# Kernel optimization log

Hardware: AMD Instinct MI355X
Metric: run time of the kernel (lower is better)

## Reference

```python
import jax, jax.numpy as jnp
import numpy as np

N_NODES = 50000
N_EDGES = 1600000
N_GRAPHS = 128
DIM_IN = 128
DIM_SELF = 16


def setup_inputs() -> dict:
    key = jax.random.key(0)
    ks = jax.random.split(key, 12)
    feat = jax.random.normal(ks[0], (N_NODES, DIM_IN), dtype=jnp.float32)
    self_feat = jax.random.normal(ks[1], (N_GRAPHS, DIM_SELF), dtype=jnp.float32)
    src = jax.random.randint(ks[2], (N_EDGES,), 0, N_NODES)
    dst = jax.random.randint(ks[3], (N_EDGES,), 0, N_NODES)
    graph_id = jnp.sort(jax.random.randint(ks[4], (N_NODES,), 0, N_GRAPHS))
    def lin(k, fan_in, fan_out):
        bound = 1.0 / np.sqrt(fan_in)
        return jax.random.uniform(k, (fan_in, fan_out), dtype=jnp.float32, minval=-bound, maxval=bound)
    W1 = lin(ks[5], DIM_IN, 100)
    b1 = jnp.zeros((100,), jnp.float32)
    W2 = lin(ks[6], 100, 20)
    b2 = jnp.zeros((20,), jnp.float32)
    Wf1 = lin(ks[7], 20 + DIM_SELF, 10)
    bf1 = jnp.zeros((10,), jnp.float32)
    Wf2 = lin(ks[8], 10, 1)
    bf2 = jnp.zeros((1,), jnp.float32)
    return {"feat": feat, "self_feat": self_feat, "src": src, "dst": dst,
            "graph_id": graph_id, "W1": W1, "b1": b1, "W2": W2, "b2": b2,
            "Wf1": Wf1, "bf1": bf1, "Wf2": Wf2, "bf2": bf2}


def _gcn_layer(h, src, dst, deg, W, b):
    # copy_u gather over edges + mean segment reduce over dst, then linear apply
    msg_sum = jax.ops.segment_sum(h[src], dst, num_segments=h.shape[0])  # [N, d]
    mean = msg_sum / jnp.maximum(deg, 1.0)[:, None]
    # DGL update_all leaves zero-in-degree nodes with their prior feature
    h_agg = jnp.where((deg > 0)[:, None], mean, h)
    return h_agg @ W + b


def reference(feat, self_feat, src, dst, graph_id, W1, b1, W2, b2, Wf1, bf1, Wf2, bf2):
    n = feat.shape[0]
    deg = jax.ops.segment_sum(jnp.ones((src.shape[0],), feat.dtype), dst, num_segments=n)
    h = jax.nn.relu(_gcn_layer(feat, src, dst, deg, W1, b1))   # [N,100]
    h = jax.nn.relu(_gcn_layer(h, src, dst, deg, W2, b2))      # [N,20]
    # dgl.mean_nodes: per-graph mean of node features
    g_sum = jax.ops.segment_sum(h, graph_id, num_segments=N_GRAPHS)  # [G,20]
    g_cnt = jax.ops.segment_sum(jnp.ones((n,), h.dtype), graph_id, num_segments=N_GRAPHS)
    hg = g_sum / jnp.maximum(g_cnt, 1.0)[:, None]
    fused = jnp.concatenate([hg, self_feat], axis=1)           # [G, 20+dim_self]
    out = jax.nn.relu(fused @ Wf1 + bf1) @ Wf2 + bf2           # [G, dim_out]
    return out
```

## Files before the change

kernel.cpp:

```cpp
#include <hip/hip_runtime.h>

constexpr int NN = 50000;
constexpr int NE = 1600000;
constexpr int NG = 128;
constexpr int BSTRIDE = 96;

constexpr int FILL_PASSES = 8;
constexpr int NODES_PER_PASS = 6250;
constexpr int BLOCKS_PER_PASS = (NE + 255) / 256;

constexpr int G1M_BLOCKS = (NN + 63) / 64;

constexpr int A1_NODES = 16;
constexpr int A1_BLOCKS = NN / A1_NODES;
constexpr int A2_BLOCKS = NN / 16;

#define OFF_CNT      0
#define OFF_GSUM     200000
#define OFF_GCNT     210240
#define ZERO_BYTES   210752
#define OFF_ADJ      210752
#define OFF_X1F      9810816
#define OFF_X2B      16210816

typedef float v2f __attribute__((ext_vector_type(2)));
typedef short bf16x8 __attribute__((ext_vector_type(8)));
typedef float f32x4 __attribute__((ext_vector_type(4)));

__device__ __forceinline__ unsigned short f2bf(float x) {
    unsigned int v = __float_as_uint(x);
    return (unsigned short)((v + 0x7FFFu + ((v >> 16) & 1u)) >> 16);
}
__device__ __forceinline__ float bflo(unsigned int u) { return __uint_as_float(u << 16); }
__device__ __forceinline__ float bfhi(unsigned int u) { return __uint_as_float(u & 0xFFFF0000u); }

__global__ void k_fill(const int* __restrict__ src, const int* __restrict__ dst,
                       int* __restrict__ cnt, unsigned short* __restrict__ adj) {
    const int pass = blockIdx.x & 7;
    const int chunk = blockIdx.x >> 3;
    const int i = chunk * 256 + threadIdx.x;
    if (i >= NE) return;
    const int d = dst[i];
    const int lo = pass * NODES_PER_PASS;
    if (d >= lo && d < lo + NODES_PER_PASS) {
        const int p = atomicAdd(&cnt[d], 1);
        if (p < BSTRIDE) adj[d * BSTRIDE + p] = (unsigned short)src[i];
    }
}

__global__ __launch_bounds__(256) void k_gemm1m(const float* __restrict__ feat,
                                                const float* __restrict__ W1,
                                                unsigned int* __restrict__ X1f) {
    const int t = threadIdx.x;
    const int wv = t >> 6;
    const int l  = t & 63;
    const int ln16 = l & 15;
    const int lh   = l >> 4;
    const int node = blockIdx.x * 64 + wv * 16 + ln16;
    const bool live = (node < NN);

    bf16x8 bfr[4];
#pragma unroll
    for (int ks = 0; ks < 4; ++ks) {
        float4 f0 = {0.f,0.f,0.f,0.f}, f1 = {0.f,0.f,0.f,0.f};
        if (live) {
            f0 = *(const float4*)(feat + node * 128 + ks * 32 + lh * 8);
            f1 = *(const float4*)(feat + node * 128 + ks * 32 + lh * 8 + 4);
        }
        bf16x8 b;
        b[0] = (short)f2bf(f0.x); b[1] = (short)f2bf(f0.y);
        b[2] = (short)f2bf(f0.z); b[3] = (short)f2bf(f0.w);
        b[4] = (short)f2bf(f1.x); b[5] = (short)f2bf(f1.y);
        b[6] = (short)f2bf(f1.z); b[7] = (short)f2bf(f1.w);
        bfr[ks] = b;
    }

#pragma unroll
    for (int ct = 0; ct < 7; ++ct) {
        const int col = ct * 16 + ln16;
        f32x4 acc = {0.f, 0.f, 0.f, 0.f};
#pragma unroll
        for (int ks = 0; ks < 4; ++ks) {
            bf16x8 a;
#pragma unroll
            for (int j = 0; j < 8; ++j) {
                const int k = ks * 32 + lh * 8 + j;
                a[j] = (col < 100) ? (short)f2bf(W1[k * 100 + col]) : (short)0;
            }
            acc = __builtin_amdgcn_mfma_f32_16x16x32_bf16(a, bfr[ks], acc, 0, 0, 0);
        }
        if (live) {
            int u = 0;
            u = __builtin_amdgcn_cvt_pk_fp8_f32(acc[0], acc[1], u, false);
            u = __builtin_amdgcn_cvt_pk_fp8_f32(acc[2], acc[3], u, true);
            X1f[node * 32 + ct * 4 + lh] = (unsigned int)u;
        }
    }
    if (live) X1f[node * 32 + 28 + lh] = 0u;
}

__global__ __launch_bounds__(256) void k_agg1g2(
        const uint4* __restrict__ X1u, const int* __restrict__ cnt,
        const unsigned short* __restrict__ adj, const float* __restrict__ b1,
        const float* __restrict__ W2, unsigned int* __restrict__ X2b) {
    __shared__ float hl[A1_NODES * 100];
    __shared__ float w2s[100 * 20];
    const int t = threadIdx.x;
    const int node0 = blockIdx.x * A1_NODES;
    for (int i = t; i < 2000; i += 256) w2s[i] = W2[i];

    const int nl   = t >> 4;
    const int l    = t & 15;
    const int q    = l & 7;
    const int half = l >> 3;
    const int node = node0 + nl;
    const int d = cnt[node];
    const unsigned short* ab = adj + node * BSTRIDE;
    float a[16];
#pragma unroll
    for (int j = 0; j < 16; ++j) a[j] = 0.f;

#define ACC4(UU, B) { v2f l_ = __builtin_amdgcn_cvt_pk_f32_fp8((int)(UU), false); \
                      v2f h_ = __builtin_amdgcn_cvt_pk_f32_fp8((int)(UU), true);  \
                      a[B+0] += l_.x; a[B+1] += l_.y; a[B+2] += h_.x; a[B+3] += h_.y; }
#define SET4(UU, B) { v2f l_ = __builtin_amdgcn_cvt_pk_f32_fp8((int)(UU), false); \
                      v2f h_ = __builtin_amdgcn_cvt_pk_f32_fp8((int)(UU), true);  \
                      a[B+0] = l_.x; a[B+1] = l_.y; a[B+2] = h_.x; a[B+3] = h_.y; }
#define ACCU4(U) ACC4((U).x, 0) ACC4((U).y, 4) ACC4((U).z, 8) ACC4((U).w, 12)

    if (q < 7) {
        if (d == 0) {
            if (half == 0) {
                const uint4 u = X1u[node * 8 + q];
                SET4(u.x, 0) SET4(u.y, 4) SET4(u.z, 8) SET4(u.w, 12)
            }
        } else {
            const int m  = (d >> 1) & ~3;
            const int i0 = half ? m : 0;
            const int i1 = half ? d : m;
            int i = i0;
            for (; i + 8 <= i1; i += 8) {
                const ushort4 sa = *(const ushort4*)(ab + i);
                const ushort4 sb = *(const ushort4*)(ab + i + 4);
                const uint4 u0 = X1u[(int)sa.x * 8 + q];
                const uint4 u1 = X1u[(int)sa.y * 8 + q];
                const uint4 u2 = X1u[(int)sa.z * 8 + q];
                const uint4 u3 = X1u[(int)sa.w * 8 + q];
                const uint4 u4 = X1u[(int)sb.x * 8 + q];
                const uint4 u5 = X1u[(int)sb.y * 8 + q];
                const uint4 u6 = X1u[(int)sb.z * 8 + q];
                const uint4 u7 = X1u[(int)sb.w * 8 + q];
                ACCU4(u0) ACCU4(u1) ACCU4(u2) ACCU4(u3)
                ACCU4(u4) ACCU4(u5) ACCU4(u6) ACCU4(u7)
            }
            for (; i + 4 <= i1; i += 4) {
                const ushort4 s4 = *(const ushort4*)(ab + i);
                const uint4 u0 = X1u[(int)s4.x * 8 + q];
                const uint4 u1 = X1u[(int)s4.y * 8 + q];
                const uint4 u2 = X1u[(int)s4.z * 8 + q];
                const uint4 u3 = X1u[(int)s4.w * 8 + q];
                ACCU4(u0) ACCU4(u1) ACCU4(u2) ACCU4(u3)
            }
            for (; i < i1; ++i) {
                const uint4 u = X1u[(int)ab[i] * 8 + q];
                ACCU4(u)
            }
        }
    }
#undef ACCU4
#undef ACC4
#undef SET4
#pragma unroll
    for (int j = 0; j < 16; ++j) a[j] += __shfl_xor(a[j], 8);

    if (half == 0 && q < 7) {
        if (d > 0) {
            const float inv = 1.f / (float)d;
#pragma unroll
            for (int j = 0; j < 16; ++j) a[j] *= inv;
        }
        const int col0 = 16 * q;
        float* hrow = hl + nl * 100 + col0;
        const int nc = (q < 6) ? 16 : 4;
#pragma unroll 4
        for (int j = 0; j < nc; ++j)
            hrow[j] = fmaxf(a[j] + b1[col0 + j], 0.f);
    }
    __syncthreads();

    const int nl2 = t >> 4;
    const int j = t & 15;
    unsigned int o = 0u;
    if (j < 10) {
        const float* h = hl + nl2 * 100;
        float a0 = 0.f, a1 = 0.f;
#pragma unroll 5
        for (int k = 0; k < 100; ++k) {
            const float hv = h[k];
            a0 += hv * w2s[k * 20 + 2 * j];
            a1 += hv * w2s[k * 20 + 2 * j + 1];
        }
        o = (unsigned int)f2bf(a0) | ((unsigned int)f2bf(a1) << 16);
    }
    X2b[(node0 + nl2) * 16 + j] = o;
}

__global__ __launch_bounds__(256) void k_agg2(const uint2* __restrict__ X2v,
                                              const int* __restrict__ cnt,
                                              const unsigned short* __restrict__ adj,
                                              const float* __restrict__ b2,
                                              const int* __restrict__ graph_id,
                                              float* __restrict__ g_sum,
                                              float* __restrict__ g_cnt) {
    __shared__ float lsum[NG * 20];
    __shared__ float lcnt[NG];
    const int t = threadIdx.x;
    for (int i = t; i < NG * 20; i += 256) lsum[i] = 0.f;
    if (t < NG) lcnt[t] = 0.f;
    __syncthreads();

    const int nl   = t >> 4;
    const int l    = t & 15;
    const int q    = l & 7;
    const int half = l >> 3;
    const int node = blockIdx.x * 16 + nl;
    const int d = cnt[node];
    const unsigned short* ab = adj + node * BSTRIDE;
    float ax = 0.f, ay = 0.f, az = 0.f, aw = 0.f;
#define ACCU2(U) { ax += bflo((U).x); ay += bfhi((U).x); \
                   az += bflo((U).y); aw += bfhi((U).y); }
    if (q < 5) {
        if (d == 0) {
            if (half == 0) {
                const uint2 u = X2v[node * 8 + q];
                ax = bflo(u.x); ay = bfhi(u.x);
                az = bflo(u.y); aw = bfhi(u.y);
            }
        } else {
            const int m  = (d >> 1) & ~3;
            const int i0 = half ? m : 0;
            const int i1 = half ? d : m;
            int i = i0;
            for (; i + 8 <= i1; i += 8) {
                const ushort4 sa = *(const ushort4*)(ab + i);
                const ushort4 sb = *(const ushort4*)(ab + i + 4);
                const uint2 u0 = X2v[(int)sa.x * 8 + q];
                const uint2 u1 = X2v[(int)sa.y * 8 + q];
                const uint2 u2 = X2v[(int)sa.z * 8 + q];
                const uint2 u3 = X2v[(int)sa.w * 8 + q];
                const uint2 u4 = X2v[(int)sb.x * 8 + q];
                const uint2 u5 = X2v[(int)sb.y * 8 + q];
                const uint2 u6 = X2v[(int)sb.z * 8 + q];
                const uint2 u7 = X2v[(int)sb.w * 8 + q];
                ACCU2(u0) ACCU2(u1) ACCU2(u2) ACCU2(u3)
                ACCU2(u4) ACCU2(u5) ACCU2(u6) ACCU2(u7)
            }
            for (; i + 4 <= i1; i += 4) {
                const ushort4 s4 = *(const ushort4*)(ab + i);
                const uint2 u0 = X2v[(int)s4.x * 8 + q];
                const uint2 u1 = X2v[(int)s4.y * 8 + q];
                const uint2 u2 = X2v[(int)s4.z * 8 + q];
                const uint2 u3 = X2v[(int)s4.w * 8 + q];
                ACCU2(u0) ACCU2(u1) ACCU2(u2) ACCU2(u3)
            }
            for (; i < i1; ++i) {
                const uint2 u = X2v[(int)ab[i] * 8 + q];
                ACCU2(u)
            }
        }
    }
#undef ACCU2
    ax += __shfl_xor(ax, 8);
    ay += __shfl_xor(ay, 8);
    az += __shfl_xor(az, 8);
    aw += __shfl_xor(aw, 8);

    if (half == 0 && q < 5) {
        if (d > 0) {
            const float inv = 1.f / (float)d;
            ax *= inv; ay *= inv; az *= inv; aw *= inv;
        }
        const int col0 = 4 * q;
        const float hx = fmaxf(ax + b2[col0 + 0], 0.f);
        const float hy = fmaxf(ay + b2[col0 + 1], 0.f);
        const float hz = fmaxf(az + b2[col0 + 2], 0.f);
        const float hw = fmaxf(aw + b2[col0 + 3], 0.f);
        const int g = graph_id[node];
        atomicAdd(&lsum[g * 20 + col0 + 0], hx);
        atomicAdd(&lsum[g * 20 + col0 + 1], hy);
        atomicAdd(&lsum[g * 20 + col0 + 2], hz);
        atomicAdd(&lsum[g * 20 + col0 + 3], hw);
    }
    if (l == 0) atomicAdd(&lcnt[graph_id[node]], 1.f);
    __syncthreads();

    const int first = blockIdx.x * 16;
    const int gmin = graph_id[first];
    const int span = graph_id[first + 15] - gmin + 1;
    for (int idx = t; idx < span * 20; idx += 256) {
        const int g = gmin + idx / 20;
        const int c = idx - (idx / 20) * 20;
        const float v = lsum[g * 20 + c];
        if (v != 0.f) atomicAdd(&g_sum[g * 20 + c], v);
    }
    for (int idx = t; idx < span; idx += 256) {
        const float v = lcnt[gmin + idx];
        if (v != 0.f) atomicAdd(&g_cnt[gmin + idx], v);
    }
}

__global__ __launch_bounds__(128) void k_final(const float* __restrict__ g_sum,
                                               const float* __restrict__ g_cnt,
                                               const float* __restrict__ self_feat,
                                               const float* __restrict__ Wf1,
                                               const float* __restrict__ bf1,
                                               const float* __restrict__ Wf2,
                                               const float* __restrict__ bf2,
                                               float* __restrict__ out) {
    const int g = threadIdx.x;
    float fused[36];
    const float cnt = fmaxf(g_cnt[g], 1.f);
    const float inv = 1.f / cnt;
#pragma unroll
    for (int j = 0; j < 20; ++j) fused[j] = g_sum[g * 20 + j] * inv;
#pragma unroll
    for (int j = 0; j < 16; ++j) fused[20 + j] = self_feat[g * 16 + j];
    float o = bf2[0];
#pragma unroll
    for (int i = 0; i < 10; ++i) {
        float t = bf1[i];
#pragma unroll
        for (int k = 0; k < 36; ++k) t += fused[k] * Wf1[k * 10 + i];
        o += fmaxf(t, 0.f) * Wf2[i];
    }
    out[g] = o;
}

extern "C" void kernel_launch(void* const* d_in, const int* in_sizes, int n_in,
                              void* d_out, int out_size, void* d_ws, size_t ws_size,
                              hipStream_t stream) {
    const float* feat      = (const float*)d_in[0];
    const float* self_feat = (const float*)d_in[1];
    const int*   src       = (const int*)d_in[2];
    const int*   dst       = (const int*)d_in[3];
    const int*   graph_id  = (const int*)d_in[4];
    const float* W1        = (const float*)d_in[5];
    const float* b1        = (const float*)d_in[6];
    const float* W2        = (const float*)d_in[7];
    const float* b2        = (const float*)d_in[8];
    const float* Wf1       = (const float*)d_in[9];
    const float* bf1       = (const float*)d_in[10];
    const float* Wf2       = (const float*)d_in[11];
    const float* bf2       = (const float*)d_in[12];

    char* w = (char*)d_ws;
    int*            cnt      = (int*)(w + OFF_CNT);
    float*          g_sum    = (float*)(w + OFF_GSUM);
    float*          g_cnt    = (float*)(w + OFF_GCNT);
    unsigned short* adj      = (unsigned short*)(w + OFF_ADJ);
    unsigned int*   X1f      = (unsigned int*)(w + OFF_X1F);
    unsigned int*   X2b      = (unsigned int*)(w + OFF_X2B);

    hipMemsetAsync(w, 0, ZERO_BYTES, stream);

    k_fill<<<FILL_PASSES * BLOCKS_PER_PASS, 256, 0, stream>>>(src, dst, cnt, adj);
    k_gemm1m<<<G1M_BLOCKS, 256, 0, stream>>>(feat, W1, X1f);
    k_agg1g2<<<A1_BLOCKS, 256, 0, stream>>>((const uint4*)X1f, cnt, adj, b1,
                                            W2, X2b);
    k_agg2<<<A2_BLOCKS, 256, 0, stream>>>((const uint2*)X2b, cnt,
                                          adj, b2, graph_id, g_sum, g_cnt);
    k_final<<<1, 128, 0, stream>>>(g_sum, g_cnt, self_feat, Wf1, bf1, Wf2, bf2,
                                   (float*)d_out);
}
```

Before: 263.4 us.

## Fuse adjacency fill with first GEMM and precompute packed bf16 W1 fragments

Merges the edge-bucketing fill kernel and the first-layer GEMM into one launch, interleaving one GEMM super-block after every 64 fill super-blocks so the compute-bound MFMA work overlaps the atomic-heavy fill. A new tiny kernel converts W1 to bf16 once and stores it in MFMA fragment order, so each GEMM wave loads ready fragments instead of gathering and converting W1 per block. This adds an extra launch and an integer divide per block, and the interleave ratio is hand-tuned.

After: 260.2 us. About the same (-1.2%).

```diff
diff --git a/kernel.cpp b/kernel.cpp
--- a/kernel.cpp
+++ b/kernel.cpp
@@ -7,9 +7,12 @@
 
 constexpr int FILL_PASSES = 8;
 constexpr int NODES_PER_PASS = 6250;
-constexpr int BLOCKS_PER_PASS = (NE + 255) / 256;
-
-constexpr int G1M_BLOCKS = (NN + 63) / 64;
+constexpr int FILL_CHUNKS = 6250;
+constexpr int G1_PERIOD = 65;
+constexpr int G1_SLOT = 32;
+constexpr int G1M_VBLOCKS = 782;
+constexpr int TOTAL_SUPERS = 6348;
+constexpr int FUSED_BLOCKS = TOTAL_SUPERS * 8;
 
 constexpr int A1_NODES = 16;
 constexpr int A1_BLOCKS = NN / A1_NODES;
@@ -22,6 +25,7 @@
 #define OFF_ADJ      210752
 #define OFF_X1F      9810816
 #define OFF_X2B      16210816
+#define OFF_W1B      19410816
 
 typedef float v2f __attribute__((ext_vector_type(2)));
 typedef short bf16x8 __attribute__((ext_vector_type(8)));
@@ -34,29 +38,62 @@
 __device__ __forceinline__ float bflo(unsigned int u) { return __uint_as_float(u << 16); }
 __device__ __forceinline__ float bfhi(unsigned int u) { return __uint_as_float(u & 0xFFFF0000u); }
 
-__global__ void k_fill(const int* __restrict__ src, const int* __restrict__ dst,
-                       int* __restrict__ cnt, unsigned short* __restrict__ adj) {
-    const int pass = blockIdx.x & 7;
-    const int chunk = blockIdx.x >> 3;
-    const int i = chunk * 256 + threadIdx.x;
-    if (i >= NE) return;
-    const int d = dst[i];
-    const int lo = pass * NODES_PER_PASS;
-    if (d >= lo && d < lo + NODES_PER_PASS) {
-        const int p = atomicAdd(&cnt[d], 1);
-        if (p < BSTRIDE) adj[d * BSTRIDE + p] = (unsigned short)src[i];
-    }
-}
-
-__global__ __launch_bounds__(256) void k_gemm1m(const float* __restrict__ feat,
-                                                const float* __restrict__ W1,
-                                                unsigned int* __restrict__ X1f) {
+__global__ __launch_bounds__(256) void k_prepw(const float* __restrict__ W1,
+                                               uint4* __restrict__ w1b) {
+    const int t = threadIdx.x;
+    const int l = t & 63;
+    const int ln16 = l & 15;
+    const int lh = l >> 4;
+    for (int fs = t >> 6; fs < 28; fs += 4) {
+        const int ct = fs >> 2;
+        const int ks = fs & 3;
+        const int col = ct * 16 + ln16;
+        unsigned short r[8];
+#pragma unroll
+        for (int j = 0; j < 8; ++j) {
+            const int k = ks * 32 + lh * 8 + j;
+            r[j] = (col < 100) ? f2bf(W1[k * 100 + col]) : (unsigned short)0;
+        }
+        uint4 u;
+        u.x = (unsigned)r[0] | ((unsigned)r[1] << 16);
+        u.y = (unsigned)r[2] | ((unsigned)r[3] << 16);
+        u.z = (unsigned)r[4] | ((unsigned)r[5] << 16);
+        u.w = (unsigned)r[6] | ((unsigned)r[7] << 16);
+        w1b[fs * 64 + l] = u;
+    }
+}
+
+__global__ __launch_bounds__(256) void k_fill_gemm1m(
+        const int* __restrict__ src, const int* __restrict__ dst,
+        int* __restrict__ cnt, unsigned short* __restrict__ adj,
+        const float* __restrict__ feat, const bf16x8* __restrict__ w1b,
+        unsigned int* __restrict__ X1f) {
+    const unsigned int super = blockIdx.x >> 3;
+    const unsigned int lane8 = blockIdx.x & 7;
+    const unsigned int qq = super / G1_PERIOD;
+    const unsigned int rr = super - qq * G1_PERIOD;
+
+    if (rr != G1_SLOT) {
+        const int chunk = (int)(super - qq - (rr > G1_SLOT ? 1u : 0u));
+        if (chunk >= FILL_CHUNKS) return;
+        const int i = chunk * 256 + threadIdx.x;
+        const int d = dst[i];
+        const int lo = (int)lane8 * NODES_PER_PASS;
+        if (d >= lo && d < lo + NODES_PER_PASS) {
+            const int p = atomicAdd(&cnt[d], 1);
+            if (p < BSTRIDE) adj[d * BSTRIDE + p] = (unsigned short)src[i];
+        }
+        return;
+    }
+
+    const int gb = (int)(qq * 8 + lane8);
+    if (gb >= G1M_VBLOCKS) return;
     const int t = threadIdx.x;
     const int wv = t >> 6;
     const int l  = t & 63;
     const int ln16 = l & 15;
     const int lh   = l >> 4;
-    const int node = blockIdx.x * 64 + wv * 16 + ln16;
+    const int node = gb * 64 + wv * 16 + ln16;
     const bool live = (node < NN);
 
     bf16x8 bfr[4];
@@ -77,16 +114,10 @@
 
 #pragma unroll
     for (int ct = 0; ct < 7; ++ct) {
-        const int col = ct * 16 + ln16;
         f32x4 acc = {0.f, 0.f, 0.f, 0.f};
 #pragma unroll
         for (int ks = 0; ks < 4; ++ks) {
-            bf16x8 a;
-#pragma unroll
-            for (int j = 0; j < 8; ++j) {
-                const int k = ks * 32 + lh * 8 + j;
-                a[j] = (col < 100) ? (short)f2bf(W1[k * 100 + col]) : (short)0;
-            }
+            const bf16x8 a = w1b[(ct * 4 + ks) * 64 + l];
             acc = __builtin_amdgcn_mfma_f32_16x16x32_bf16(a, bfr[ks], acc, 0, 0, 0);
         }
         if (live) {
@@ -360,11 +391,13 @@
     unsigned short* adj      = (unsigned short*)(w + OFF_ADJ);
     unsigned int*   X1f      = (unsigned int*)(w + OFF_X1F);
     unsigned int*   X2b      = (unsigned int*)(w + OFF_X2B);
+    uint4*          w1b      = (uint4*)(w + OFF_W1B);
 
     hipMemsetAsync(w, 0, ZERO_BYTES, stream);
 
-    k_fill<<<FILL_PASSES * BLOCKS_PER_PASS, 256, 0, stream>>>(src, dst, cnt, adj);
-    k_gemm1m<<<G1M_BLOCKS, 256, 0, stream>>>(feat, W1, X1f);
+    k_prepw<<<1, 256, 0, stream>>>(W1, w1b);
+    k_fill_gemm1m<<<FUSED_BLOCKS, 256, 0, stream>>>(src, dst, cnt, adj, feat,
+                                                    (const bf16x8*)w1b, X1f);
     k_agg1g2<<<A1_BLOCKS, 256, 0, stream>>>((const uint4*)X1f, cnt, adj, b1,
                                             W2, X2b);
     k_agg2<<<A2_BLOCKS, 256, 0, stream>>>((const uint2*)X2b, cnt,
```
